# Performance work log

Hardware: AMD Instinct MI355X
Metric: run time of the kernel (lower is better)

Reference implementation:

```python
import jax, jax.numpy as jnp
import numpy as np

K = 20          # neighbors
NEG = 0.2       # LeakyReLU slope


def _edge_block(feat, W, s, b):
    """EdgeConv: knn -> edge feature gather -> 1x1 conv (W) -> BN affine (s,b)
    -> LeakyReLU -> max over k.  feat: (B,N,C) -> (B,N,Cout)."""
    sq = jnp.sum(feat * feat, axis=-1, keepdims=True)            # (B,N,1)
    dist = sq + jnp.swapaxes(sq, 1, 2) - 2.0 * jnp.einsum('bnc,bmc->bnm', feat, feat)
    dist = jnp.maximum(dist, 0.0)
    _, idx = jax.lax.top_k(-dist, K)                             # (B,N,K) smallest dists
    nbr = jax.vmap(lambda f, i: f[i])(feat, idx)                 # (B,N,K,C) gather
    ctr = jnp.broadcast_to(feat[:, :, None, :], nbr.shape)
    edge = jnp.concatenate([nbr - ctr, ctr], axis=-1)            # (B,N,K,2C)
    h = jnp.einsum('bnkc,oc->bnko', edge, W)                     # 1x1 conv, no bias
    h = jax.nn.leaky_relu(h * s + b, NEG)                        # eval-mode BN folded to affine
    return jnp.max(h, axis=2)                                    # max over k neighbors


def setup_inputs() -> dict:
    key = jax.random.key(0)
    ks = jax.random.split(key, 32)
    B, N = 8, 2048
    d = {}
    d['x'] = jax.random.normal(ks[0], (B, 3, N), dtype=jnp.float32)
    # EdgeConv 1x1 conv weights (Cout, Cin) and folded BN affine (scale, bias)
    chans = [(6, 64), (2 * 67, 64), (2 * 131, 64), (2 * 195, 128), (323, 1024)]
    for i, (cin, cout) in enumerate(chans, start=1):
        d[f'W{i}'] = 0.1 * jax.random.normal(ks[3 * i], (cout, cin), dtype=jnp.float32)
        d[f's{i}'] = 1.0 + 0.1 * jax.random.normal(ks[3 * i + 1], (cout,), dtype=jnp.float32)
        d[f'b{i}'] = 0.1 * jax.random.normal(ks[3 * i + 2], (cout,), dtype=jnp.float32)
    # FC head: fc1 1024->512 (+BN), fc2 512->256 (+BN), fc3 256->40
    d['fW1'] = 0.05 * jax.random.normal(ks[20], (512, 1024), dtype=jnp.float32)
    d['fb1'] = 0.05 * jax.random.normal(ks[21], (512,), dtype=jnp.float32)
    d['fs1'] = 1.0 + 0.1 * jax.random.normal(ks[22], (512,), dtype=jnp.float32)
    d['fB1'] = 0.1 * jax.random.normal(ks[23], (512,), dtype=jnp.float32)
    d['fW2'] = 0.05 * jax.random.normal(ks[24], (256, 512), dtype=jnp.float32)
    d['fb2'] = 0.05 * jax.random.normal(ks[25], (256,), dtype=jnp.float32)
    d['fs2'] = 1.0 + 0.1 * jax.random.normal(ks[26], (256,), dtype=jnp.float32)
    d['fB2'] = 0.1 * jax.random.normal(ks[27], (256,), dtype=jnp.float32)
    d['fW3'] = 0.05 * jax.random.normal(ks[28], (40, 256), dtype=jnp.float32)
    d['fb3'] = 0.05 * jax.random.normal(ks[29], (40,), dtype=jnp.float32)
    return d


def reference(x, W1, s1, b1, W2, s2, b2, W3, s3, b3, W4, s4, b4, W5, s5, b5,
              fW1, fb1, fs1, fB1, fW2, fb2, fs2, fB2, fW3, fb3):
    pts = jnp.swapaxes(x, 1, 2)                                  # (B,N,3)
    f1 = _edge_block(pts, W1, s1, b1)                            # (B,N,64)
    x2 = jnp.concatenate([pts, f1], axis=-1)
    f2 = _edge_block(x2, W2, s2, b2)                             # (B,N,64)
    x3 = jnp.concatenate([pts, f1, f2], axis=-1)
    f3 = _edge_block(x3, W3, s3, b3)                             # (B,N,64)
    x4 = jnp.concatenate([pts, f1, f2, f3], axis=-1)
    f4 = _edge_block(x4, W4, s4, b4)                             # (B,N,128)
    g = jnp.concatenate([pts, f1, f2, f3, f4], axis=-1)          # (B,N,323)
    g = jax.nn.leaky_relu(jnp.einsum('bnc,oc->bno', g, W5) * s5 + b5, NEG)
    gfeat = jnp.max(g, axis=1)                                   # (B,1024) global max pool
    h = jax.nn.leaky_relu((gfeat @ fW1.T + fb1) * fs1 + fB1, NEG)  # dropout=eval noop
    h = jax.nn.leaky_relu((h @ fW2.T + fb2) * fs2 + fB2, NEG)
    logits = h @ fW3.T + fb3                                     # (B,40)
    return logits, gfeat
```

## Files before the change

### kernel.cpp

```cpp
#include <hip/hip_runtime.h>
#include <math.h>


constexpr int BB = 8;
constexpr int NN = 2048;
constexpr int KK = 20;
constexpr int CT = 323;
constexpr int XS = 324;
constexpr int X4S = XS / 4;
constexpr float NEGS = 0.2f;

__device__ __forceinline__ float lrelu(float v) { return v > 0.0f ? v : NEGS * v; }

__device__ __forceinline__ void atomicMaxF(float* addr, float v) {
    if (v >= 0.0f) atomicMax((int*)addr, __float_as_int(v));
    else           atomicMin((unsigned int*)addr, __float_as_uint(v));
}

__device__ __forceinline__ void fma4(float4& a, float x, const float4 w) {
    a.x = fmaf(x, w.x, a.x); a.y = fmaf(x, w.y, a.y);
    a.z = fmaf(x, w.z, a.z); a.w = fmaf(x, w.w, a.w);
}

constexpr int WTOT = 19072;
__global__ void k_prep_all(const float* __restrict__ W1, const float* __restrict__ W2,
                           const float* __restrict__ W3, const float* __restrict__ W4,
                           const float* __restrict__ W5, const float* __restrict__ x,
                           float4* __restrict__ WT4, float* __restrict__ W5T,
                           float* __restrict__ gfeat, float* __restrict__ X,
                           float* __restrict__ sq) {
    int j = blockIdx.x * blockDim.x + threadIdx.x;
    if (j < WTOT) {
        int base, Cout, C;
        const float* W;
        if (j < 128)       { base = 0;    Cout = 64;  C = 3;   W = W1; }
        else if (j < 2304) { base = 128;  Cout = 64;  C = 67;  W = W2; }
        else if (j < 6528) { base = 2304; Cout = 64;  C = 131; W = W3; }
        else               { base = 6528; Cout = 128; C = 195; W = W4; }
        int W4w = Cout / 2;
        int local = j - base;
        int c = local / W4w, og = local - c * W4w;
        float v[4];
#pragma unroll
        for (int q = 0; q < 4; ++q) {
            int o2 = 4 * og + q;
            if (c >= C) v[q] = 0.f;
            else if (o2 < Cout) v[q] = W[(size_t)o2 * 2 * C + c];
            else {
                int o = o2 - Cout;
                v[q] = W[(size_t)o * 2 * C + C + c] - W[(size_t)o * 2 * C + c];
            }
        }
        WT4[j] = make_float4(v[0], v[1], v[2], v[3]);
    } else if (j < WTOT + XS * 1024) {
        int t = j - WTOT;
        int c = t / 1024, o = t % 1024;
        W5T[t] = (c < CT) ? W5[(size_t)o * CT + c] : 0.f;
    } else if (j < WTOT + XS * 1024 + BB * 1024) {
        gfeat[j - WTOT - XS * 1024] = -INFINITY;
    } else if (j < WTOT + XS * 1024 + BB * 1024 + BB * NN) {
        int i = j - WTOT - XS * 1024 - BB * 1024;
        int b = i >> 11, n = i & 2047;
        const float* xb = x + (size_t)b * 3 * NN;
        float vx = xb[n], vy = xb[NN + n], vz = xb[2 * NN + n];
        float* row = X + (size_t)i * XS;
        row[0] = vx; row[1] = vy; row[2] = vz; row[3] = 0.f;
        sq[i] = vx * vx + vy * vy + vz * vz;
    } else if (j < WTOT + XS * 1024 + BB * 1024 + BB * NN + BB * NN * 80) {
        int t = j - (WTOT + XS * 1024 + BB * 1024 + BB * NN);
        int row = t / 80, c4 = 1 + (t - 80 * row);
        ((float4*)X)[(size_t)row * X4S + c4] = make_float4(0.f, 0.f, 0.f, 0.f);
    }
}

constexpr int TM = 128;
__global__ __launch_bounds__(256) void k_dist(const float* __restrict__ X,
                                              const float* __restrict__ sq,
                                              float* __restrict__ dist, int C) {
    int b = blockIdx.z;
    int blk = blockIdx.x;
    int ti = (int)((sqrtf(8.0f * blk + 1.0f) - 1.0f) * 0.5f);
    while ((ti + 1) * (ti + 2) / 2 <= blk) ++ti;
    while (ti * (ti + 1) / 2 > blk) --ti;
    int tj = blk - ti * (ti + 1) / 2;
    int m0 = ti * TM;
    int n0 = tj * TM;
    __shared__ float smem[4352];
    float* AsB = smem;
    float* BsB = smem + 2048;
    int tid = threadIdx.x;
    int tx = tid & 15;
    int ty = tid >> 4;
    float acc[8][8] = {};
    const float* Xb = X + (size_t)b * NN * XS;
    int sr = tid & 127;
    int sc0 = (tid >> 7) * 8;
    for (int c0 = 0; c0 < C; c0 += 16) {
        const float* arow = Xb + (size_t)(n0 + sr) * XS + c0 + sc0;
        const float* brow = Xb + (size_t)(m0 + sr) * XS + c0 + sc0;
        float4 a0 = *(const float4*)(arow);
        float4 a1 = *(const float4*)(arow + 4);
        float4 b0 = *(const float4*)(brow);
        float4 b1 = *(const float4*)(brow + 4);
        float av[8] = {a0.x, a0.y, a0.z, a0.w, a1.x, a1.y, a1.z, a1.w};
        float bv8[8] = {b0.x, b0.y, b0.z, b0.w, b1.x, b1.y, b1.z, b1.w};
#pragma unroll
        for (int i = 0; i < 8; ++i) {
            bool inr = (c0 + sc0 + i) < C;
            AsB[(sc0 + i) * TM + sr] = inr ? av[i] : 0.f;
            BsB[(sc0 + i) * TM + sr] = inr ? bv8[i] : 0.f;
        }
        __syncthreads();
#pragma unroll
        for (int cc = 0; cc < 16; ++cc) {
            float4 a0r = *(const float4*)&AsB[cc * TM + ty * 8];
            float4 a1r = *(const float4*)&AsB[cc * TM + ty * 8 + 4];
            float a[8] = {a0r.x, a0r.y, a0r.z, a0r.w, a1r.x, a1r.y, a1r.z, a1r.w};
            float4 b0r = *(const float4*)&BsB[cc * TM + tx * 4];
            float4 b1r = *(const float4*)&BsB[cc * TM + 64 + tx * 4];
            float bv[8] = {b0r.x, b0r.y, b0r.z, b0r.w, b1r.x, b1r.y, b1r.z, b1r.w};
#pragma unroll
            for (int i = 0; i < 8; ++i)
#pragma unroll
                for (int j = 0; j < 8; ++j)
                    acc[i][j] = fmaf(a[i], bv[j], acc[i][j]);
        }
        __syncthreads();
    }
    const float* sqb = sq + b * NN;
    float* db = dist + (size_t)b * NN * NN;
    float sm[8];
#pragma unroll
    for (int j = 0; j < 8; ++j) sm[j] = sqb[m0 + (j >> 2) * 64 + tx * 4 + (j & 3)];
#pragma unroll
    for (int i = 0; i < 8; ++i) {
        int n = n0 + ty * 8 + i;
        float sn = sqb[n];
#pragma unroll
        for (int j = 0; j < 8; ++j) {
            float d = fmaxf(sn + sm[j] - 2.f * acc[i][j], 0.f);
            acc[i][j] = d;
        }
        *(float4*)&db[(size_t)n * NN + m0 + tx * 4] =
            make_float4(acc[i][0], acc[i][1], acc[i][2], acc[i][3]);
        *(float4*)&db[(size_t)n * NN + m0 + 64 + tx * 4] =
            make_float4(acc[i][4], acc[i][5], acc[i][6], acc[i][7]);
    }
    if (ti != tj) {
        float* T = smem;
        int r = tid >> 3;
        int c0r = (tid & 7) * 16;
#pragma unroll
        for (int h = 0; h < 2; ++h) {
#pragma unroll
            for (int p2 = 0; p2 < 2; ++p2) {
                __syncthreads();
                if ((tx >> 3) == p2) {
#pragma unroll
                    for (int jj = 0; jj < 4; ++jj)
#pragma unroll
                        for (int i = 0; i < 8; ++i)
                            T[((tx & 7) * 4 + jj) * 129 + ty * 8 + i] = acc[i][h * 4 + jj];
                }
                __syncthreads();
                float v[16];
#pragma unroll
                for (int k = 0; k < 16; ++k) v[k] = T[r * 129 + c0r + k];
                float* dst = db + (size_t)(m0 + h * 64 + 32 * p2 + r) * NN + n0 + c0r;
#pragma unroll
                for (int k = 0; k < 4; ++k)
                    *(float4*)(dst + 4 * k) = make_float4(v[4 * k], v[4 * k + 1],
                                                          v[4 * k + 2], v[4 * k + 3]);
            }
        }
    }
}

__global__ __launch_bounds__(128) void k_select(const float* __restrict__ dist,
                                                int* __restrict__ idx) {
    int bn = blockIdx.x;
    int tid = threadIdx.x;
    int wv = tid >> 6;
    int lane = tid & 63;
    const float* drow = dist + (size_t)bn * NN;
    int m0 = tid * 16;
    unsigned long long keys[16];
#pragma unroll
    for (int i = 0; i < 4; ++i) {
        float4 v = *(const float4*)(drow + m0 + 4 * i);
        keys[4 * i + 0] = ((unsigned long long)__float_as_uint(v.x) << 11) | (unsigned)(m0 + 4 * i + 0);
        keys[4 * i + 1] = ((unsigned long long)__float_as_uint(v.y) << 11) | (unsigned)(m0 + 4 * i + 1);
        keys[4 * i + 2] = ((unsigned long long)__float_as_uint(v.z) << 11) | (unsigned)(m0 + 4 * i + 2);
        keys[4 * i + 3] = ((unsigned long long)__float_as_uint(v.w) << 11) | (unsigned)(m0 + 4 * i + 3);
    }
    unsigned long long mn = keys[0];
#pragma unroll
    for (int i = 1; i < 16; ++i) mn = keys[i] < mn ? keys[i] : mn;
    unsigned long long mx = mn;
#pragma unroll
    for (int s = 1; s < 64; s <<= 1) {
        unsigned long long o = (unsigned long long)__shfl_xor((long long)mx, s, 64);
        mx = o > mx ? o : mx;
    }
    __shared__ unsigned long long sB[2];
    __shared__ unsigned long long sT;
    __shared__ int sWant;
    __shared__ int sCnt;
    __shared__ int hist[256];
    if (lane == 0) sB[wv] = mx;
    if (tid == 0) { sT = 0ull; sWant = KK; sCnt = 0; }
    __syncthreads();
    unsigned long long B = sB[0] < sB[1] ? sB[0] : sB[1];
#pragma unroll 1
    for (int level = 0; level < 6; ++level) {
        int sh = 40 - 8 * level;
        hist[tid] = 0; hist[tid + 128] = 0;
        __syncthreads();
        unsigned long long pref = sT;
#pragma unroll
        for (int i = 0; i < 16; ++i) {
            unsigned long long k = keys[i];
            if (k <= B && (k >> (sh + 8)) == (pref >> (sh + 8)))
                atomicAdd(&hist[(int)((k >> sh) & 255)], 1);
        }
        __syncthreads();
        if (tid < 64) {
            int h0 = hist[4 * tid], h1 = hist[4 * tid + 1];
            int h2 = hist[4 * tid + 2], h3 = hist[4 * tid + 3];
            int s = h0 + h1 + h2 + h3;
            int inc = s;
#pragma unroll
            for (int d = 1; d < 64; d <<= 1) {
                int o = __shfl_up(inc, d, 64);
                if (lane >= d) inc += o;
            }
            int want = sWant;
            int c = inc - s;
            int bsel = -1, rem = 0;
            if (c < want && want <= c + h0) { bsel = 4 * tid + 0; rem = want - c; } c += h0;
            if (bsel < 0 && c < want && want <= c + h1) { bsel = 4 * tid + 1; rem = want - c; } c += h1;
            if (bsel < 0 && c < want && want <= c + h2) { bsel = 4 * tid + 2; rem = want - c; } c += h2;
            if (bsel < 0 && c < want && want <= c + h3) { bsel = 4 * tid + 3; rem = want - c; }
            if (bsel >= 0) {
                sT = pref | ((unsigned long long)bsel << sh);
                sWant = rem;
            }
        }
        __syncthreads();
    }
    unsigned long long T = sT;
    int* orow = idx + (size_t)bn * KK;
#pragma unroll
    for (int i = 0; i < 16; ++i) {
        if (keys[i] <= T) {
            int s = atomicAdd(&sCnt, 1);
            orow[s] = (int)(keys[i] & 2047u);
        }
    }
}

template <int KC4, int COUT>
__global__ __launch_bounds__(256)
void k_hg(const float* __restrict__ X, const float4* __restrict__ WT4,
          float* __restrict__ H, float* __restrict__ G) {
    constexpr int W4 = COUT / 2;
    constexpr int RB2 = 32;
    constexpr int RPT = RB2 * W4 / 256;
    int bn0 = blockIdx.x * RB2;
    __shared__ float4 xs[RB2][KC4];
    int tid = threadIdx.x;
    const float4* X4 = (const float4*)X;
    for (int j = tid; j < RB2 * KC4; j += 256) {
        int r = j / KC4, c = j - r * KC4;
        xs[r][c] = X4[(size_t)(bn0 + r) * X4S + c];
    }
    __syncthreads();
    int og = tid & (W4 - 1);
    int rg = tid / W4;
    float4 acc[RPT];
#pragma unroll
    for (int i = 0; i < RPT; ++i) acc[i] = make_float4(0.f, 0.f, 0.f, 0.f);
#pragma unroll 2
    for (int c4 = 0; c4 < KC4; ++c4) {
        float4 w0 = WT4[(size_t)(4 * c4 + 0) * W4 + og];
        float4 w1 = WT4[(size_t)(4 * c4 + 1) * W4 + og];
        float4 w2 = WT4[(size_t)(4 * c4 + 2) * W4 + og];
        float4 w3 = WT4[(size_t)(4 * c4 + 3) * W4 + og];
#pragma unroll
        for (int i = 0; i < RPT; ++i) {
            float4 xv = xs[rg * RPT + i][c4];
            fma4(acc[i], xv.x, w0);
            fma4(acc[i], xv.y, w1);
            fma4(acc[i], xv.z, w2);
            fma4(acc[i], xv.w, w3);
        }
    }
    int o2 = 4 * og;
#pragma unroll
    for (int i = 0; i < RPT; ++i) {
        int bn = bn0 + rg * RPT + i;
        if (o2 < COUT) *(float4*)&H[(size_t)bn * COUT + o2] = acc[i];
        else           *(float4*)&G[(size_t)bn * COUT + (o2 - COUT)] = acc[i];
    }
}

template <int COUT>
__global__ __launch_bounds__(256)
void k_edgemax(const float* __restrict__ H, const float* __restrict__ G,
               const int* __restrict__ idx, const float* __restrict__ scale,
               const float* __restrict__ bias, int outoff,
               float* __restrict__ X, float* __restrict__ sq) {
    constexpr int CPL = COUT / 64;
    int wv = threadIdx.x >> 6, lane = threadIdx.x & 63;
    int bn = blockIdx.x * 4 + wv;
    int b = bn >> 11;
    int id = idx[(size_t)bn * KK + (lane < KK ? lane : 0)];
    float gv[CPL], sv[CPL], bv[CPL], mx[CPL];
#pragma unroll
    for (int q = 0; q < CPL; ++q) {
        int o = lane + 64 * q;
        gv[q] = G[(size_t)bn * COUT + o];
        sv[q] = scale[o];
        bv[q] = bias[o];
        mx[q] = -INFINITY;
    }
#pragma unroll
    for (int k = 0; k < KK; ++k) {
        int m = __shfl(id, k, 64);
        const float* hrow = H + (size_t)(b * NN + m) * COUT;
#pragma unroll
        for (int q = 0; q < CPL; ++q) {
            float v = hrow[lane + 64 * q] + gv[q];
            mx[q] = fmaxf(mx[q], lrelu(v * sv[q] + bv[q]));
        }
    }
    float* orow = X + (size_t)bn * XS + outoff;
    float v = 0.f;
#pragma unroll
    for (int q = 0; q < CPL; ++q) {
        orow[lane + 64 * q] = mx[q];
        v = fmaf(mx[q], mx[q], v);
    }
#pragma unroll
    for (int s = 1; s < 64; s <<= 1) v += __shfl_xor(v, s, 64);
    if (lane == 0) sq[bn] += v;
}

constexpr int RB = 32;
__global__ __launch_bounds__(512) void k_stage5(const float* __restrict__ X,
                                                const float* __restrict__ W5T,
                                                const float* __restrict__ s5,
                                                const float* __restrict__ b5,
                                                float* __restrict__ gfeat) {
    int blk = blockIdx.x;
    int b = blk / (NN / RB);
    int n0 = (blk % (NN / RB)) * RB;
    int tid = threadIdx.x;
    const float4* X4 = (const float4*)X;
    const float4* W5T4 = (const float4*)W5T;
    int og = tid & 255;
    int r0 = __builtin_amdgcn_readfirstlane((tid >> 8) * 16);
    const float4* xrows = X4 + (size_t)(b * NN + n0 + r0) * X4S;
    float acc[16][4] = {};
    for (int c4 = 0; c4 < X4S; ++c4) {
        float4 w0 = W5T4[(size_t)(4 * c4 + 0) * 256 + og];
        float4 w1 = W5T4[(size_t)(4 * c4 + 1) * 256 + og];
        float4 w2 = W5T4[(size_t)(4 * c4 + 2) * 256 + og];
        float4 w3 = W5T4[(size_t)(4 * c4 + 3) * 256 + og];
#pragma unroll
        for (int r = 0; r < 16; ++r) {
            float4 a = xrows[(size_t)r * X4S + c4];
            acc[r][0] = fmaf(a.x, w0.x, acc[r][0]);
            acc[r][1] = fmaf(a.x, w0.y, acc[r][1]);
            acc[r][2] = fmaf(a.x, w0.z, acc[r][2]);
            acc[r][3] = fmaf(a.x, w0.w, acc[r][3]);
            acc[r][0] = fmaf(a.y, w1.x, acc[r][0]);
            acc[r][1] = fmaf(a.y, w1.y, acc[r][1]);
            acc[r][2] = fmaf(a.y, w1.z, acc[r][2]);
            acc[r][3] = fmaf(a.y, w1.w, acc[r][3]);
            acc[r][0] = fmaf(a.z, w2.x, acc[r][0]);
            acc[r][1] = fmaf(a.z, w2.y, acc[r][1]);
            acc[r][2] = fmaf(a.z, w2.z, acc[r][2]);
            acc[r][3] = fmaf(a.z, w2.w, acc[r][3]);
            acc[r][0] = fmaf(a.w, w3.x, acc[r][0]);
            acc[r][1] = fmaf(a.w, w3.y, acc[r][1]);
            acc[r][2] = fmaf(a.w, w3.z, acc[r][2]);
            acc[r][3] = fmaf(a.w, w3.w, acc[r][3]);
        }
    }
    int o0 = og * 4;
#pragma unroll
    for (int i = 0; i < 4; ++i) {
        int o = o0 + i;
        float s = s5[o], bbv = b5[o];
        float mx = -INFINITY;
#pragma unroll
        for (int r = 0; r < 16; ++r) {
            float v = lrelu(acc[r][i] * s + bbv);
            mx = fmaxf(v, mx);
        }
        atomicMaxF(&gfeat[b * 1024 + o], mx);
    }
}

__global__ __launch_bounds__(256) void k_fc(const float* __restrict__ gfeat,
                                            const float* __restrict__ fW1, const float* __restrict__ fb1,
                                            const float* __restrict__ fs1, const float* __restrict__ fB1,
                                            const float* __restrict__ fW2, const float* __restrict__ fb2,
                                            const float* __restrict__ fs2, const float* __restrict__ fB2,
                                            const float* __restrict__ fW3, const float* __restrict__ fb3,
                                            float* __restrict__ logits) {
    int b = blockIdx.x;
    __shared__ float g[1024];
    __shared__ float h1s[512];
    __shared__ float h2s[256];
    int tid = threadIdx.x;
    for (int j = tid; j < 1024; j += 256) g[j] = gfeat[b * 1024 + j];
    __syncthreads();
    for (int o = tid; o < 512; o += 256) {
        const float* wr = fW1 + (size_t)o * 1024;
        float acc = 0.f;
        for (int c = 0; c < 1024; ++c) acc = fmaf(g[c], wr[c], acc);
        h1s[o] = lrelu((acc + fb1[o]) * fs1[o] + fB1[o]);
    }
    __syncthreads();
    {
        int o = tid;
        const float* wr = fW2 + (size_t)o * 512;
        float acc = 0.f;
        for (int c = 0; c < 512; ++c) acc = fmaf(h1s[c], wr[c], acc);
        h2s[o] = lrelu((acc + fb2[o]) * fs2[o] + fB2[o]);
    }
    __syncthreads();
    if (tid < 40) {
        const float* wr = fW3 + (size_t)tid * 256;
        float acc = 0.f;
        for (int c = 0; c < 256; ++c) acc = fmaf(h2s[c], wr[c], acc);
        logits[b * 40 + tid] = acc + fb3[tid];
    }
}

extern "C" void kernel_launch(void* const* d_in, const int* in_sizes, int n_in,
                              void* d_out, int out_size, void* d_ws, size_t ws_size,
                              hipStream_t stream) {
    const float* x   = (const float*)d_in[0];
    const float* W1  = (const float*)d_in[1];
    const float* s1  = (const float*)d_in[2];
    const float* b1  = (const float*)d_in[3];
    const float* W2  = (const float*)d_in[4];
    const float* s2  = (const float*)d_in[5];
    const float* b2  = (const float*)d_in[6];
    const float* W3  = (const float*)d_in[7];
    const float* s3  = (const float*)d_in[8];
    const float* b3  = (const float*)d_in[9];
    const float* W4  = (const float*)d_in[10];
    const float* s4  = (const float*)d_in[11];
    const float* b4  = (const float*)d_in[12];
    const float* W5  = (const float*)d_in[13];
    const float* s5  = (const float*)d_in[14];
    const float* b5  = (const float*)d_in[15];
    const float* fW1 = (const float*)d_in[16];
    const float* fb1 = (const float*)d_in[17];
    const float* fs1 = (const float*)d_in[18];
    const float* fB1 = (const float*)d_in[19];
    const float* fW2 = (const float*)d_in[20];
    const float* fb2 = (const float*)d_in[21];
    const float* fs2 = (const float*)d_in[22];
    const float* fB2 = (const float*)d_in[23];
    const float* fW3 = (const float*)d_in[24];
    const float* fb3 = (const float*)d_in[25];

    float* out    = (float*)d_out;
    float* logits = out;
    float* gfeat  = out + 320;

    char* ws = (char*)d_ws;
    size_t off = 0;
    auto alloc = [&](size_t bytes) -> void* {
        void* p = ws + off;
        off += (bytes + 255) & ~(size_t)255;
        return p;
    };
    float* X    = (float*)alloc((size_t)BB * NN * XS * 4);
    float* sq   = (float*)alloc((size_t)BB * NN * 4);
    float* dist = (float*)alloc((size_t)BB * NN * NN * 4);
    int*   idx  = (int*)  alloc((size_t)BB * NN * KK * 4);
    float4* WT4 = (float4*)alloc((size_t)WTOT * 16);
    float* H    = (float*)alloc((size_t)BB * NN * 128 * 4);
    float* G    = (float*)alloc((size_t)BB * NN * 128 * 4);
    float* W5T  = (float*)alloc((size_t)XS * 1024 * 4);
    (void)ws_size; (void)in_sizes; (void)n_in; (void)out_size;

    int prepTot = WTOT + XS * 1024 + BB * 1024 + BB * NN + BB * NN * 80;
    k_prep_all<<<(prepTot + 255) / 256, 256, 0, stream>>>(W1, W2, W3, W4, W5, x,
                                                          WT4, W5T, gfeat, X, sq);

    const int Cs[4]    = {3, 67, 131, 195};
    const int offs[4]  = {3, 67, 131, 195};
    const int WOFF[4]  = {0, 128, 2304, 6528};
    const float* ss[4] = {s1, s2, s3, s4};
    const float* bs[4] = {b1, b2, b3, b4};

    constexpr int NT = NN / TM;
    constexpr int NBLK = NT * (NT + 1) / 2;
    for (int st = 0; st < 4; ++st) {
        int C = Cs[st];
        dim3 dg(NBLK, 1, BB);
        k_dist<<<dg, 256, 0, stream>>>(X, sq, dist, C);
        k_select<<<BB * NN, 128, 0, stream>>>(dist, idx);
        const float4* wt = WT4 + WOFF[st];
        switch (st) {
            case 0:
                k_hg<1, 64><<<BB * NN / 32, 256, 0, stream>>>(X, wt, H, G);
                k_edgemax<64><<<BB * NN / 4, 256, 0, stream>>>(H, G, idx, ss[st], bs[st], offs[st], X, sq);
                break;
            case 1:
                k_hg<17, 64><<<BB * NN / 32, 256, 0, stream>>>(X, wt, H, G);
                k_edgemax<64><<<BB * NN / 4, 256, 0, stream>>>(H, G, idx, ss[st], bs[st], offs[st], X, sq);
                break;
            case 2:
                k_hg<33, 64><<<BB * NN / 32, 256, 0, stream>>>(X, wt, H, G);
                k_edgemax<64><<<BB * NN / 4, 256, 0, stream>>>(H, G, idx, ss[st], bs[st], offs[st], X, sq);
                break;
            case 3:
                k_hg<49, 128><<<BB * NN / 32, 256, 0, stream>>>(X, wt, H, G);
                k_edgemax<128><<<BB * NN / 4, 256, 0, stream>>>(H, G, idx, ss[st], bs[st], offs[st], X, sq);
                break;
        }
    }

    k_stage5<<<BB * (NN / RB), 512, 0, stream>>>(X, W5T, s5, b5, gfeat);
    k_fc<<<BB, 256, 0, stream>>>(gfeat, fW1, fb1, fs1, fB1,
                                 fW2, fb2, fs2, fB2, fW3, fb3, logits);
}
```

Baseline: 1.011 ms.

## Rewrite k-NN select as single-wave radix select with compacted candidates

Result: slower. 1.067 ms (+5.6%).

```diff
diff --git a/kernel.cpp b/kernel.cpp
--- a/kernel.cpp
+++ b/kernel.cpp
@@ -176,86 +176,124 @@
     }
 }
 
-__global__ __launch_bounds__(128) void k_select(const float* __restrict__ dist,
-                                                int* __restrict__ idx) {
+__global__ __launch_bounds__(64) void k_select(const float* __restrict__ dist,
+                                               int* __restrict__ idx) {
     int bn = blockIdx.x;
-    int tid = threadIdx.x;
-    int wv = tid >> 6;
-    int lane = tid & 63;
+    int lane = threadIdx.x;
     const float* drow = dist + (size_t)bn * NN;
-    int m0 = tid * 16;
-    unsigned long long keys[16];
-#pragma unroll
-    for (int i = 0; i < 4; ++i) {
+    int m0 = lane * 32;
+    unsigned long long lanebelow = (1ull << lane) - 1ull;
+    unsigned long long mn = ~0ull;
+#pragma unroll
+    for (int i = 0; i < 8; ++i) {
         float4 v = *(const float4*)(drow + m0 + 4 * i);
-        keys[4 * i + 0] = ((unsigned long long)__float_as_uint(v.x) << 11) | (unsigned)(m0 + 4 * i + 0);
-        keys[4 * i + 1] = ((unsigned long long)__float_as_uint(v.y) << 11) | (unsigned)(m0 + 4 * i + 1);
-        keys[4 * i + 2] = ((unsigned long long)__float_as_uint(v.z) << 11) | (unsigned)(m0 + 4 * i + 2);
-        keys[4 * i + 3] = ((unsigned long long)__float_as_uint(v.w) << 11) | (unsigned)(m0 + 4 * i + 3);
-    }
-    unsigned long long mn = keys[0];
-#pragma unroll
-    for (int i = 1; i < 16; ++i) mn = keys[i] < mn ? keys[i] : mn;
-    unsigned long long mx = mn;
+        unsigned long long k0 = ((unsigned long long)__float_as_uint(v.x) << 11) | (unsigned)(m0 + 4 * i + 0);
+        unsigned long long k1 = ((unsigned long long)__float_as_uint(v.y) << 11) | (unsigned)(m0 + 4 * i + 1);
+        unsigned long long k2 = ((unsigned long long)__float_as_uint(v.z) << 11) | (unsigned)(m0 + 4 * i + 2);
+        unsigned long long k3 = ((unsigned long long)__float_as_uint(v.w) << 11) | (unsigned)(m0 + 4 * i + 3);
+        mn = k0 < mn ? k0 : mn; mn = k1 < mn ? k1 : mn;
+        mn = k2 < mn ? k2 : mn; mn = k3 < mn ? k3 : mn;
+    }
+    unsigned long long B = mn;
 #pragma unroll
     for (int s = 1; s < 64; s <<= 1) {
-        unsigned long long o = (unsigned long long)__shfl_xor((long long)mx, s, 64);
-        mx = o > mx ? o : mx;
-    }
-    __shared__ unsigned long long sB[2];
-    __shared__ unsigned long long sT;
-    __shared__ int sWant;
-    __shared__ int sCnt;
+        unsigned long long o = (unsigned long long)__shfl_xor((long long)B, s, 64);
+        B = o > B ? o : B;
+    }
+    __shared__ unsigned long long sKeys[2048];
+    __shared__ unsigned long long sSmall[8];
     __shared__ int hist[256];
-    if (lane == 0) sB[wv] = mx;
-    if (tid == 0) { sT = 0ull; sWant = KK; sCnt = 0; }
-    __syncthreads();
-    unsigned long long B = sB[0] < sB[1] ? sB[0] : sB[1];
+    int base = 0;
+#pragma unroll
+    for (int i = 0; i < 8; ++i) {
+        float4 v = *(const float4*)(drow + m0 + 4 * i);
+        unsigned long long kk[4];
+        kk[0] = ((unsigned long long)__float_as_uint(v.x) << 11) | (unsigned)(m0 + 4 * i + 0);
+        kk[1] = ((unsigned long long)__float_as_uint(v.y) << 11) | (unsigned)(m0 + 4 * i + 1);
+        kk[2] = ((unsigned long long)__float_as_uint(v.z) << 11) | (unsigned)(m0 + 4 * i + 2);
+        kk[3] = ((unsigned long long)__float_as_uint(v.w) << 11) | (unsigned)(m0 + 4 * i + 3);
+#pragma unroll
+        for (int q = 0; q < 4; ++q) {
+            bool p = kk[q] <= B;
+            unsigned long long bal = __ballot(p);
+            if (p) {
+                int off = __popcll(bal & lanebelow);
+                sKeys[base + off] = kk[q];
+            }
+            base += __popcll(bal);
+        }
+    }
+    int nS = base;
+    __builtin_amdgcn_wave_barrier();
+    unsigned long long T = 0;
+    int want = KK;
 #pragma unroll 1
     for (int level = 0; level < 6; ++level) {
         int sh = 40 - 8 * level;
-        hist[tid] = 0; hist[tid + 128] = 0;
-        __syncthreads();
-        unsigned long long pref = sT;
-#pragma unroll
-        for (int i = 0; i < 16; ++i) {
-            unsigned long long k = keys[i];
-            if (k <= B && (k >> (sh + 8)) == (pref >> (sh + 8)))
+        hist[lane] = 0; hist[lane + 64] = 0; hist[lane + 128] = 0; hist[lane + 192] = 0;
+        __builtin_amdgcn_wave_barrier();
+        for (int j = lane; j < nS; j += 64) {
+            unsigned long long k = sKeys[j];
+            if ((k >> (sh + 8)) == (T >> (sh + 8)))
                 atomicAdd(&hist[(int)((k >> sh) & 255)], 1);
         }
-        __syncthreads();
-        if (tid < 64) {
-            int h0 = hist[4 * tid], h1 = hist[4 * tid + 1];
-            int h2 = hist[4 * tid + 2], h3 = hist[4 * tid + 3];
-            int s = h0 + h1 + h2 + h3;
-            int inc = s;
-#pragma unroll
-            for (int d = 1; d < 64; d <<= 1) {
-                int o = __shfl_up(inc, d, 64);
-                if (lane >= d) inc += o;
+        __builtin_amdgcn_wave_barrier();
+        int h0 = hist[4 * lane], h1 = hist[4 * lane + 1];
+        int h2 = hist[4 * lane + 2], h3 = hist[4 * lane + 3];
+        int s = h0 + h1 + h2 + h3;
+        int inc = s;
+#pragma unroll
+        for (int d = 1; d < 64; d <<= 1) {
+            int o = __shfl_up(inc, d, 64);
+            if (lane >= d) inc += o;
+        }
+        int c = inc - s;
+        int bsel = -1, rem = 0, bcnt = 0;
+        if (c < want && want <= c + h0) { bsel = 4 * lane + 0; rem = want - c; bcnt = h0; } c += h0;
+        if (bsel < 0 && c < want && want <= c + h1) { bsel = 4 * lane + 1; rem = want - c; bcnt = h1; } c += h1;
+        if (bsel < 0 && c < want && want <= c + h2) { bsel = 4 * lane + 2; rem = want - c; bcnt = h2; } c += h2;
+        if (bsel < 0 && c < want && want <= c + h3) { bsel = 4 * lane + 3; rem = want - c; bcnt = h3; }
+        unsigned long long balv = __ballot(bsel >= 0);
+        int src = (int)(__ffsll((unsigned long long)balv) - 1);
+        unsigned long long Tn = T | ((unsigned long long)(bsel < 0 ? 0 : bsel) << sh);
+        T    = (unsigned long long)__shfl((long long)Tn, src, 64);
+        want = __shfl(rem, src, 64);
+        bcnt = __shfl(bcnt, src, 64);
+        if (bcnt <= 8) {
+            int gb = 0;
+            int nSpad = (nS + 63) & ~63;
+            for (int j = lane; j < nSpad; j += 64) {
+                bool p = (j < nS) && ((sKeys[j] >> sh) == (T >> sh));
+                unsigned long long bal2 = __ballot(p);
+                if (p) {
+                    int off = __popcll(bal2 & lanebelow);
+                    sSmall[gb + off] = sKeys[j];
+                }
+                gb += __popcll(bal2);
             }
-            int want = sWant;
-            int c = inc - s;
-            int bsel = -1, rem = 0;
-            if (c < want && want <= c + h0) { bsel = 4 * tid + 0; rem = want - c; } c += h0;
-            if (bsel < 0 && c < want && want <= c + h1) { bsel = 4 * tid + 1; rem = want - c; } c += h1;
-            if (bsel < 0 && c < want && want <= c + h2) { bsel = 4 * tid + 2; rem = want - c; } c += h2;
-            if (bsel < 0 && c < want && want <= c + h3) { bsel = 4 * tid + 3; rem = want - c; }
-            if (bsel >= 0) {
-                sT = pref | ((unsigned long long)bsel << sh);
-                sWant = rem;
-            }
-        }
-        __syncthreads();
-    }
-    unsigned long long T = sT;
+            __builtin_amdgcn_wave_barrier();
+            unsigned long long myk = (lane < bcnt) ? sSmall[lane] : ~0ull;
+            int rank = 0;
+#pragma unroll 1
+            for (int j = 0; j < bcnt; ++j) rank += (sSmall[j] <= myk) ? 1 : 0;
+            bool win = (lane < bcnt) && (rank == want);
+            unsigned long long balw = __ballot(win);
+            int srcw = (int)(__ffsll((unsigned long long)balw) - 1);
+            T = (unsigned long long)__shfl((long long)myk, srcw, 64);
+            break;
+        }
+    }
     int* orow = idx + (size_t)bn * KK;
-#pragma unroll
-    for (int i = 0; i < 16; ++i) {
-        if (keys[i] <= T) {
-            int s = atomicAdd(&sCnt, 1);
-            orow[s] = (int)(keys[i] & 2047u);
-        }
+    int eb = 0;
+    int nSpad = (nS + 63) & ~63;
+    for (int j = lane; j < nSpad; j += 64) {
+        bool p = (j < nS) && (sKeys[j] <= T);
+        unsigned long long bal3 = __ballot(p);
+        if (p) {
+            int off = __popcll(bal3 & lanebelow);
+            orow[eb + off] = (int)(sKeys[j] & 2047u);
+        }
+        eb += __popcll(bal3);
     }
 }
 
@@ -507,7 +545,7 @@
         int C = Cs[st];
         dim3 dg(NBLK, 1, BB);
         k_dist<<<dg, 256, 0, stream>>>(X, sq, dist, C);
-        k_select<<<BB * NN, 128, 0, stream>>>(dist, idx);
+        k_select<<<BB * NN, 64, 0, stream>>>(dist, idx);
         const float4* wt = WT4 + WOFF[st];
         switch (st) {
             case 0:
```
